# Performance work log

Hardware: AMD Instinct MI355X
Metric: run time of the kernel (lower is better)

## Reference

```python
import jax, jax.numpy as jnp
import numpy as np

B, T, S, D, V = 8, 64, 512, 512, 50000


def setup_inputs() -> dict:
    key = jax.random.key(0)
    k1, k2, k3, k4, k5 = jax.random.split(key, 5)
    x = jax.random.normal(k1, (B, T, D), dtype=jnp.float32)
    attn_dist = jax.random.normal(k2, (B, T, S), dtype=jnp.float32)
    enc_batch_extend_vocab = jax.random.randint(k3, (B, S), 0, V, dtype=jnp.int64)
    W_proj = jax.random.normal(k4, (D, V), dtype=jnp.float32) * (1.0 / np.sqrt(D))
    b_proj = jnp.zeros((V,), dtype=jnp.float32)
    W_pgen = jax.random.normal(k5, (D, 1), dtype=jnp.float32) * (1.0 / np.sqrt(D))
    b_pgen = jnp.zeros((1,), dtype=jnp.float32)
    return {"x": x, "attn_dist": attn_dist,
            "enc_batch_extend_vocab": enc_batch_extend_vocab,
            "W_proj": W_proj, "b_proj": b_proj,
            "W_pgen": W_pgen, "b_pgen": b_pgen}


def reference(x, attn_dist, enc_batch_extend_vocab, W_proj, b_proj, W_pgen, b_pgen):
    # pointer-generator head, temp=1, beam_search=False
    temp = 1.0
    # p_gen gate: [B, T, 1]
    alpha = jax.nn.sigmoid(jnp.einsum('btd,de->bte', x, W_pgen) + b_pgen)
    # vocab projection + softmax: [B, T, V]
    logit = jnp.einsum('btd,dv->btv', x, W_proj) + b_proj
    vocab_dist = jax.nn.softmax(logit / temp, axis=2)
    vocab_dist_ = alpha * vocab_dist
    # copy distribution over source positions: [B, T, S]
    attn = jax.nn.softmax(attn_dist / temp, axis=-1)
    attn_ = (1.0 - alpha) * attn
    # scatter_add copy probs into vocab dim (index broadcast over T)
    b_idx = jnp.arange(B)[:, None, None]        # [B,1,1]
    t_idx = jnp.arange(T)[None, :, None]        # [1,T,1]
    v_idx = enc_batch_extend_vocab[:, None, :]  # [B,1,S]
    merged = vocab_dist_.at[b_idx, t_idx, v_idx].add(attn_)
    return jnp.log(merged)
```

## Files before the change

kernel.cpp:

```cpp
#include <hip/hip_runtime.h>
#include <math.h>
#include <stdint.h>

#define B_ 8
#define T_ 64
#define S_ 512
#define D_ 512
#define V_ 50000
#define VP_ 50176
#define M_ (B_*T_)
#define ROWB_ ((size_t)V_ * 4)

typedef __bf16 bf16_t;
typedef bf16_t bf16x8 __attribute__((ext_vector_type(8)));
typedef float  f32x4  __attribute__((ext_vector_type(4)));

__device__ inline float blk_sum(float v, float* sm) {
    #pragma unroll
    for (int o = 32; o > 0; o >>= 1) v += __shfl_down(v, o);
    int lane = threadIdx.x & 63, wid = threadIdx.x >> 6;
    __syncthreads();
    if (lane == 0) sm[wid] = v;
    __syncthreads();
    return sm[0] + sm[1] + sm[2] + sm[3];
}

__device__ inline float blk_max(float v, float* sm) {
    #pragma unroll
    for (int o = 32; o > 0; o >>= 1) v = fmaxf(v, __shfl_down(v, o));
    int lane = threadIdx.x & 63, wid = threadIdx.x >> 6;
    __syncthreads();
    if (lane == 0) sm[wid] = v;
    __syncthreads();
    return fmaxf(fmaxf(sm[0], sm[1]), fmaxf(sm[2], sm[3]));
}

__device__ inline void unpack8(uint4 u, float f[8]) {
    uint32_t w0 = u.x, w1 = u.y, w2 = u.z, w3 = u.w;
    f[0] = __uint_as_float(w0 << 16); f[1] = __uint_as_float(w0 & 0xffff0000u);
    f[2] = __uint_as_float(w1 << 16); f[3] = __uint_as_float(w1 & 0xffff0000u);
    f[4] = __uint_as_float(w2 << 16); f[5] = __uint_as_float(w2 & 0xffff0000u);
    f[6] = __uint_as_float(w3 << 16); f[7] = __uint_as_float(w3 & 0xffff0000u);
}

__global__ __launch_bounds__(256) void kprep(
    const float* __restrict__ x, const float* __restrict__ attn_dist,
    const float* __restrict__ W_pgen, const float* __restrict__ b_pgen,
    float* __restrict__ logalpha_out, float* __restrict__ attn_out, bf16_t* __restrict__ xb,
    const int* __restrict__ idx, int* __restrict__ owner_g)
{
    __shared__ int shb[S_];
    int bid = blockIdx.x;
    int tid = threadIdx.x;

    if (bid < M_) {
        float* sm = reinterpret_cast<float*>(shb);
        int row = bid;

        float2 xv = reinterpret_cast<const float2*>(x + (size_t)row * D_)[tid];
        float2 wv = reinterpret_cast<const float2*>(W_pgen)[tid];
        union { bf16_t h[2]; uint32_t u; } pk;
        pk.h[0] = (bf16_t)xv.x; pk.h[1] = (bf16_t)xv.y;
        reinterpret_cast<uint32_t*>(xb + (size_t)row * D_)[tid] = pk.u;

        float dot = blk_sum(xv.x * wv.x + xv.y * wv.y, sm);
        float alpha = 1.f / (1.f + expf(-(dot + b_pgen[0])));
        if (tid == 0) logalpha_out[row] = logf(alpha);

        float a0 = attn_dist[(size_t)row * S_ + tid];
        float a1 = attn_dist[(size_t)row * S_ + tid + 256];
        float mx = blk_max(fmaxf(a0, a1), sm);
        float e0 = expf(a0 - mx), e1 = expf(a1 - mx);
        float s = blk_sum(e0 + e1, sm);
        float scale = (1.f - alpha) / s;
        attn_out[(size_t)row * S_ + tid]       = e0 * scale;
        attn_out[(size_t)row * S_ + tid + 256] = e1 * scale;
    } else {
        int b = bid - M_;
        for (int s = tid; s < S_; s += 256) shb[s] = idx[b * S_ + s];
        __syncthreads();
        for (int s = tid; s < S_; s += 256) {
            int v = shb[s], o = s;
            for (int s2 = 0; s2 < s; s2++) if (shb[s2] == v) { o = s2; break; }
            owner_g[b * S_ + s] = o;
        }
    }
}

#define GBM 128
#define GBN 128
#define GBK 32
#define NTK_ 16
#define BP_ 132

__global__ __launch_bounds__(256) void k2_mfma(
    const bf16_t* __restrict__ A, const float* __restrict__ W,
    const float* __restrict__ bias, char* __restrict__ outB)
{
    __shared__ bf16_t As[2][GBM][GBK];
    __shared__ __attribute__((aligned(16))) float Bf[2][GBK * BP_];
    int tid  = threadIdx.x;
    int lane = tid & 63;
    int w    = tid >> 6;
    int wm   = w >> 1, wn = w & 1;

    int bid = blockIdx.x;
    int q = bid >> 5, r = bid & 31;
    int bn = (q * 8 + (r & 7)) * GBN;
    int bm = (r >> 3) * GBM;

    f32x4 acc[4][4] = {};
    float4 wreg[4];

#define STAGE_A(BUF, K0)                                                               \
    {                                                                                  \
        _Pragma("unroll")                                                              \
        for (int i = 0; i < 2; i++) {                                                  \
            int e = (w * 2 + i) * 512 + lane * 8;                                      \
            int rr_ = e >> 5, c = e & 31;                                              \
            __builtin_amdgcn_global_load_lds(                                          \
                (const __attribute__((address_space(1))) void*)                        \
                    &A[(size_t)(bm + rr_) * D_ + (K0) + c],                            \
                (__attribute__((address_space(3))) void*)&As[BUF][(w * 2 + i) * 16][0],\
                16, 0, 0);                                                             \
        }                                                                              \
    }

#define LOAD_B(K0)                                                                     \
    {                                                                                  \
        _Pragma("unroll")                                                              \
        for (int p = 0; p < 4; p++) {                                                  \
            int i = p * 256 + tid;                                        \
            int rr_ = i >> 5;                                         \
            int c4 = i & 31;                                           \
            int gv = bn + c4 * 4;                                                      \
            wreg[p] = (gv < V_) ? *reinterpret_cast<const float4*>(                    \
                                      &W[(size_t)((K0) + rr_) * V_ + gv])              \
                                : make_float4(0.f, 0.f, 0.f, 0.f);                     \
        }                                                                              \
    }

#define WRITE_B(BUF)                                                                   \
    {                                                                                  \
        _Pragma("unroll")                                                              \
        for (int p = 0; p < 4; p++) {                                                  \
            int i = p * 256 + tid;                                                     \
            int rr_ = i >> 5;                                                          \
            int c4 = i & 31;                                                           \
            int sl = c4 ^ ((rr_ >> 3) << 2);                                           \
            *reinterpret_cast<float4*>(&Bf[BUF][rr_ * BP_ + sl * 4]) = wreg[p];        \
        }                                                                              \
    }

#define COMPUTE(BUF)                                                                   \
    {                                                                                  \
        bf16x8 af[4], bfr[4];                                                          \
        int kb = (lane >> 4) * 8;                                                      \
        int key = ((kb >> 3) << 2);              \
        _Pragma("unroll")                                                              \
        for (int mi = 0; mi < 4; mi++)                                                 \
            af[mi] = *reinterpret_cast<const bf16x8*>(                                 \
                &As[BUF][wm * 64 + mi * 16 + (lane & 15)][kb]);                        \
        _Pragma("unroll")                                                              \
        for (int ni = 0; ni < 4; ni++) {                                               \
            int n = wn * 64 + ni * 16 + (lane & 15);                                   \
            int sladdr = ((n >> 2) ^ key) * 4 + (n & 3);                               \
            bf16x8 bb;                                                                 \
            _Pragma("unroll")                                                          \
            for (int j = 0; j < 8; j++)                                                \
                bb[j] = (bf16_t)Bf[BUF][(kb + j) * BP_ + sladdr];                      \
            bfr[ni] = bb;                                                              \
        }                                                                              \
        _Pragma("unroll")                                                              \
        for (int mi = 0; mi < 4; mi++)                                                 \
            _Pragma("unroll")                                                          \
            for (int ni = 0; ni < 4; ni++)                                             \
                acc[mi][ni] = __builtin_amdgcn_mfma_f32_16x16x32_bf16(af[mi], bfr[ni], acc[mi][ni], 0, 0, 0); \
    }

    LOAD_B(0);
    STAGE_A(0, 0);
    asm volatile("s_waitcnt vmcnt(0)" ::: "memory");
    WRITE_B(0);
    __syncthreads();

    #pragma unroll
    for (int tt = 0; tt < NTK_; tt++) {
        int cur = tt & 1, nxt = cur ^ 1;
        if (tt + 1 < NTK_) {
            LOAD_B((tt + 1) * GBK);
            STAGE_A(nxt, (tt + 1) * GBK);
        }
        COMPUTE(cur);
        if (tt + 1 < NTK_) {
            asm volatile("s_waitcnt vmcnt(0)" ::: "memory");
            WRITE_B(nxt);
        }
        __syncthreads();
    }
#undef STAGE_A
#undef LOAD_B
#undef WRITE_B
#undef COMPUTE

    int cm = bm + wm * 64, cn = bn + wn * 64;
    #pragma unroll
    for (int ni = 0; ni < 4; ni++) {
        int n = cn + ni * 16 + (lane & 15);
        float bv = (n < V_) ? bias[n] : 0.f;
        #pragma unroll
        for (int mi = 0; mi < 4; mi++) {
            int rbase = cm + mi * 16 + (lane >> 4) * 4;
            #pragma unroll
            for (int rr = 0; rr < 4; rr++) {
                bf16_t val = (bf16_t)(acc[mi][ni][rr] + bv);
                *reinterpret_cast<bf16_t*>(outB + (size_t)(rbase + rr) * ROWB_ + 2 * (size_t)n) = val;
            }
        }
    }
}

#define CHUNK_ 2048
#define NCH_ ((V_ + CHUNK_ - 1) / CHUNK_)

__global__ __launch_bounds__(256) void k345_final(
    char* __restrict__ outB, const float* __restrict__ attn_, const int* __restrict__ idx,
    const int* __restrict__ owner_g, const float* __restrict__ logalpha)
{
    __shared__ float att[S_];
    __shared__ int own[S_], ids[S_];
    __shared__ float smm[4], sms[4];
    int row = blockIdx.x;
    int b = row >> 6;
    int tid = threadIdx.x;
    int lane = tid & 63, wid = tid >> 6;

    for (int s = tid; s < S_; s += 256) {
        att[s] = attn_[(size_t)row * S_ + s];
        own[s] = owner_g[b * S_ + s];
        ids[s] = idx[b * S_ + s];
    }

    const uint4* L4 = reinterpret_cast<const uint4*>(outB + (size_t)row * ROWB_);
    float m = -INFINITY, se = 0.f;
    for (int i = tid; i < V_ / 8; i += 256) {
        uint4 u = L4[i];
        float f[8]; unpack8(u, f);
        float m8 = fmaxf(fmaxf(fmaxf(f[0], f[1]), fmaxf(f[2], f[3])),
                         fmaxf(fmaxf(f[4], f[5]), fmaxf(f[6], f[7])));
        float mn = fmaxf(m, m8);
        se = se * __expf(m - mn)
           + __expf(f[0] - mn) + __expf(f[1] - mn) + __expf(f[2] - mn) + __expf(f[3] - mn)
           + __expf(f[4] - mn) + __expf(f[5] - mn) + __expf(f[6] - mn) + __expf(f[7] - mn);
        m = mn;
    }
    #pragma unroll
    for (int o = 32; o > 0; o >>= 1) {
        float m2 = __shfl_down(m, o);
        float s2 = __shfl_down(se, o);
        float mn = fmaxf(m, m2);
        if (mn == -INFINITY) { se = 0.f; }
        else se = se * __expf(m - mn) + s2 * __expf(m2 - mn);
        m = mn;
    }
    __syncthreads();
    if (lane == 0) { smm[wid] = m; sms[wid] = se; }
    __syncthreads();
    float M = smm[0], Ssum = sms[0];
    #pragma unroll
    for (int wv = 1; wv < 4; wv++) {
        float m2 = smm[wv], s2 = sms[wv];
        float mn = fmaxf(M, m2);
        if (mn != -INFINITY) Ssum = Ssum * __expf(M - mn) + s2 * __expf(m2 - mn);
        M = mn;
    }
    float logden = M + logf(Ssum);
    float c_ = logalpha[row] - logden;

    for (int s = tid; s < S_; s += 256)
        if (own[s] != s) atomicAdd(&att[own[s]], att[s]);
    __syncthreads();

    const ushort* Lrow = reinterpret_cast<const ushort*>(outB + (size_t)row * ROWB_);
    float* frow = reinterpret_cast<float*>(outB + (size_t)row * ROWB_);
    for (int c = NCH_ - 1; c >= 0; c--) {
        int i0 = c * CHUNK_ + tid * 8;
        uint4 u = make_uint4(0, 0, 0, 0);
        bool act = (i0 + 8 <= V_);
        if (act) u = *reinterpret_cast<const uint4*>(Lrow + i0);
        __syncthreads();
        if (act) {
            float f[8]; unpack8(u, f);
            float4 lo = make_float4(f[0] + c_, f[1] + c_, f[2] + c_, f[3] + c_);
            float4 hi = make_float4(f[4] + c_, f[5] + c_, f[6] + c_, f[7] + c_);
            *reinterpret_cast<float4*>(frow + i0)     = lo;
            *reinterpret_cast<float4*>(frow + i0 + 4) = hi;
        }
        __syncthreads();
    }

    for (int s = tid; s < S_; s += 256) {
        if (own[s] == s) {
            int v = ids[s];
            frow[v] = logf(expf(frow[v]) + att[s]);
        }
    }
}

__global__ __launch_bounds__(256) void k1_alpha_attn(
    const float* __restrict__ x, const float* __restrict__ attn_dist,
    const float* __restrict__ W_pgen, const float* __restrict__ b_pgen,
    float* __restrict__ logalpha_out, float* __restrict__ attn_out)
{
    __shared__ float sm[4];
    int row = blockIdx.x;
    int tid = threadIdx.x;
    float2 xv = reinterpret_cast<const float2*>(x + (size_t)row * D_)[tid];
    float2 wv = reinterpret_cast<const float2*>(W_pgen)[tid];
    float dot = blk_sum(xv.x * wv.x + xv.y * wv.y, sm);
    float alpha = 1.f / (1.f + expf(-(dot + b_pgen[0])));
    if (tid == 0) logalpha_out[row] = logf(alpha);
    float a0 = attn_dist[(size_t)row * S_ + tid];
    float a1 = attn_dist[(size_t)row * S_ + tid + 256];
    float mx = blk_max(fmaxf(a0, a1), sm);
    float e0 = expf(a0 - mx), e1 = expf(a1 - mx);
    float s = blk_sum(e0 + e1, sm);
    float scale = (1.f - alpha) / s;
    attn_out[(size_t)row * S_ + tid]       = e0 * scale;
    attn_out[(size_t)row * S_ + tid + 256] = e1 * scale;
}

__global__ __launch_bounds__(512) void k5a_owner(const int* __restrict__ idx, int* __restrict__ owner_g)
{
    __shared__ int ids[S_];
    int b = blockIdx.x;
    int s = threadIdx.x;
    ids[s] = idx[b * S_ + s];
    __syncthreads();
    int v = ids[s], o = s;
    for (int s2 = 0; s2 < s; s2++) if (ids[s2] == v) { o = s2; break; }
    owner_g[b * S_ + s] = o;
}

#define BM 64
#define BN 64
#define BK 16
__global__ __launch_bounds__(256) void k2_gemm(
    const float* __restrict__ A, const float* __restrict__ W,
    const float* __restrict__ bias, float* __restrict__ C)
{
    __shared__ float As2[BK][BM + 1];
    __shared__ float Bs2[BK][BN + 1];
    int bn = blockIdx.x * BN;
    int bm = blockIdx.y * BM;
    int tid = threadIdx.x;
    int tx = tid & 15;
    int ty = tid >> 4;
    bool full_n = (bn + BN <= V_);
    float acc[4][4] = {};
    for (int k0 = 0; k0 < D_; k0 += BK) {
        {
            int i = tid * 4;
            int row = i >> 4, col = i & 15;
            const float4 av = *reinterpret_cast<const float4*>(&A[(size_t)(bm + row) * D_ + k0 + col]);
            As2[col + 0][row] = av.x; As2[col + 1][row] = av.y;
            As2[col + 2][row] = av.z; As2[col + 3][row] = av.w;
        }
        {
            int i = tid * 4;
            int row = i >> 6, col = i & 63;
            int gn = bn + col;
            if (full_n) {
                const float4 bv = *reinterpret_cast<const float4*>(&W[(size_t)(k0 + row) * V_ + gn]);
                Bs2[row][col + 0] = bv.x; Bs2[row][col + 1] = bv.y;
                Bs2[row][col + 2] = bv.z; Bs2[row][col + 3] = bv.w;
            } else {
                #pragma unroll
                for (int j = 0; j < 4; j++)
                    Bs2[row][col + j] = (gn + j < V_) ? W[(size_t)(k0 + row) * V_ + gn + j] : 0.f;
            }
        }
        __syncthreads();
        #pragma unroll
        for (int kk = 0; kk < BK; kk++) {
            float a[4], b[4];
            #pragma unroll
            for (int i = 0; i < 4; i++) a[i] = As2[kk][ty * 4 + i];
            #pragma unroll
            for (int j = 0; j < 4; j++) b[j] = Bs2[kk][tx + j * 16];
            #pragma unroll
            for (int i = 0; i < 4; i++)
                #pragma unroll
                for (int j = 0; j < 4; j++)
                    acc[i][j] += a[i] * b[j];
        }
        __syncthreads();
    }
    #pragma unroll
    for (int i = 0; i < 4; i++) {
        int m = bm + ty * 4 + i;
        #pragma unroll
        for (int j = 0; j < 4; j++) {
            int n = bn + tx + j * 16;
            if (n < V_) C[(size_t)m * V_ + n] = acc[i][j] + bias[n];
        }
    }
}

__global__ __launch_bounds__(256) void k3_stats(const float* __restrict__ C, float* __restrict__ logden)
{
    __shared__ float smm[4], sms[4];
    int row = blockIdx.x;
    const float4* p = reinterpret_cast<const float4*>(C + (size_t)row * V_);
    float m = -INFINITY, s = 0.f;
    for (int i = threadIdx.x; i < V_ / 4; i += 256) {
        float4 v = p[i];
        float m4 = fmaxf(fmaxf(v.x, v.y), fmaxf(v.z, v.w));
        if (m4 > m) { s *= expf(m - m4); m = m4; }
        s += expf(v.x - m) + expf(v.y - m) + expf(v.z - m) + expf(v.w - m);
    }
    #pragma unroll
    for (int o = 32; o > 0; o >>= 1) {
        float m2 = __shfl_down(m, o);
        float s2 = __shfl_down(s, o);
        float mn = fmaxf(m, m2);
        s = s * expf(m - mn) + s2 * expf(m2 - mn);
        m = mn;
    }
    int lane = threadIdx.x & 63, wid = threadIdx.x >> 6;
    if (lane == 0) { smm[wid] = m; sms[wid] = s; }
    __syncthreads();
    if (threadIdx.x == 0) {
        float M = smm[0], S = sms[0];
        #pragma unroll
        for (int wv = 1; wv < 4; wv++) {
            float m2 = smm[wv], s2 = sms[wv];
            float mn = fmaxf(M, m2);
            S = S * expf(M - mn) + s2 * expf(m2 - mn);
            M = mn;
        }
        logden[row] = M + logf(S);
    }
}

__global__ __launch_bounds__(256) void k4_scale(
    float* __restrict__ C, const float* __restrict__ logalpha, const float* __restrict__ logden)
{
    int row = blockIdx.y;
    int i = blockIdx.x * 256 + threadIdx.x;
    if (i >= V_ / 4) return;
    float c_ = logalpha[row] - logden[row];
    float4* p = reinterpret_cast<float4*>(C + (size_t)row * V_) + i;
    float4 v = *p;
    v.x += c_; v.y += c_; v.z += c_; v.w += c_;
    *p = v;
}

__global__ __launch_bounds__(256) void k5_scatter_log(
    float* __restrict__ C, const float* __restrict__ attn_, const int* __restrict__ idx,
    const int* __restrict__ owner_g)
{
    __shared__ float att[S_];
    __shared__ int own[S_], ids[S_];
    int row = blockIdx.x;
    int b = row >> 6;
    int tid = threadIdx.x;
    for (int s = tid; s < S_; s += 256) {
        att[s] = attn_[(size_t)row * S_ + s];
        own[s] = owner_g[b * S_ + s];
        ids[s] = idx[b * S_ + s];
    }
    __syncthreads();
    for (int s = tid; s < S_; s += 256)
        if (own[s] != s) atomicAdd(&att[own[s]], att[s]);
    __syncthreads();
    for (int s = tid; s < S_; s += 256) {
        if (own[s] == s) {
            int v = ids[s];
            float* p = &C[(size_t)row * V_ + v];
            *p = logf(expf(*p) + att[s]);
        }
    }
}

extern "C" void kernel_launch(void* const* d_in, const int* in_sizes, int n_in,
                              void* d_out, int out_size, void* d_ws, size_t ws_size,
                              hipStream_t stream) {
    const float* x         = (const float*)d_in[0];
    const float* attn_dist = (const float*)d_in[1];
    const int*   ebev      = (const int*)  d_in[2];
    const float* W_proj    = (const float*)d_in[3];
    const float* b_proj    = (const float*)d_in[4];
    const float* W_pgen    = (const float*)d_in[5];
    const float* b_pgen    = (const float*)d_in[6];
    float* out = (float*)d_out;
    char*  outB = (char*)d_out;

    float*  logalpha = (float*)d_ws;
    float*  logden   = logalpha + M_;
    float*  attn_    = logden + M_;
    int*    owner    = (int*)(attn_ + (size_t)B_ * T_ * S_);
    bf16_t* xb       = (bf16_t*)(owner + (size_t)B_ * S_);
    size_t need = (size_t)(2 * M_ + B_ * T_ * S_ + B_ * S_) * 4
                + (size_t)M_ * D_ * 2;

    if (ws_size >= need) {
        kprep<<<M_ + B_, 256, 0, stream>>>(
            x, attn_dist, W_pgen, b_pgen, logalpha, attn_, xb, ebev, owner);

        k2_mfma<<<(VP_ / GBN) * (M_ / GBM), 256, 0, stream>>>(xb, W_proj, b_proj, outB);

        k345_final<<<M_, 256, 0, stream>>>(outB, attn_, ebev, owner, logalpha);
    } else {
        k1_alpha_attn<<<M_, 256, 0, stream>>>(x, attn_dist, W_pgen, b_pgen, logalpha, attn_);
        k5a_owner<<<B_, 512, 0, stream>>>(ebev, owner);
        dim3 g2((V_ + BN - 1) / BN, M_ / BM);
        k2_gemm<<<g2, 256, 0, stream>>>(x, W_proj, b_proj, out);
        k3_stats<<<M_, 256, 0, stream>>>(out, logden);
        dim3 g4((V_ / 4 + 255) / 256, M_);
        k4_scale<<<g4, 256, 0, stream>>>(out, logalpha, logden);
        k5_scatter_log<<<M_, 256, 0, stream>>>(out, attn_, ebev, owner);
    }
}
```

Before: 186.2 us.

## Store B tile as transposed bf16 in LDS with XOR swizzle

The W tile is now converted to bf16 once when written to shared memory and stored n-major (transposed) with an XOR swizzle, instead of being kept as fp32 k-major and converted element by element in the inner compute loop. Each thread loads four consecutive k rows for the same columns so it can pack four bf16 values per 8-byte store. The compute loop reads B fragments with two 8-byte LDS loads rather than eight scalar fp32 loads plus conversions. This halves B-tile LDS footprint and cuts LDS read instructions, at the cost of narrower global load coalescing pattern and more pack work in the write stage.

```diff
diff --git a/kernel.cpp b/kernel.cpp
--- a/kernel.cpp
+++ b/kernel.cpp
@@ -91,14 +91,13 @@
 #define GBN 128
 #define GBK 32
 #define NTK_ 16
-#define BP_ 132
 
 __global__ __launch_bounds__(256) void k2_mfma(
     const bf16_t* __restrict__ A, const float* __restrict__ W,
     const float* __restrict__ bias, char* __restrict__ outB)
 {
     __shared__ bf16_t As[2][GBM][GBK];
-    __shared__ __attribute__((aligned(16))) float Bf[2][GBK * BP_];
+    __shared__ bf16_t Bs[2][GBN * GBK];
     int tid  = threadIdx.x;
     int lane = tid & 63;
     int w    = tid >> 6;
@@ -108,6 +107,11 @@
     int q = bid >> 5, r = bid & 31;
     int bn = (q * 8 + (r & 7)) * GBN;
     int bm = (r >> 3) * GBM;
+
+    int kq  = tid >> 5;
+    int c4w = tid & 31;
+    int gv  = bn + c4w * 4;
+    bool vok = (gv < V_);
 
     f32x4 acc[4][4] = {};
     float4 wreg[4];
@@ -129,26 +133,24 @@
 #define LOAD_B(K0)                                                                     \
     {                                                                                  \
         _Pragma("unroll")                                                              \
-        for (int p = 0; p < 4; p++) {                                                  \
-            int i = p * 256 + tid;                                        \
-            int rr_ = i >> 5;                                         \
-            int c4 = i & 31;                                           \
-            int gv = bn + c4 * 4;                                                      \
-            wreg[p] = (gv < V_) ? *reinterpret_cast<const float4*>(                    \
-                                      &W[(size_t)((K0) + rr_) * V_ + gv])              \
-                                : make_float4(0.f, 0.f, 0.f, 0.f);                     \
-        }                                                                              \
+        for (int p = 0; p < 4; p++)                                                    \
+            wreg[p] = vok ? *reinterpret_cast<const float4*>(                          \
+                                &W[(size_t)((K0) + kq * 4 + p) * V_ + gv])             \
+                          : make_float4(0.f, 0.f, 0.f, 0.f);                           \
     }
 
 #define WRITE_B(BUF)                                                                   \
     {                                                                                  \
+        int sl = (kq ^ (c4w & 7)) * 4;                                                 \
         _Pragma("unroll")                                                              \
-        for (int p = 0; p < 4; p++) {                                                  \
-            int i = p * 256 + tid;                                                     \
-            int rr_ = i >> 5;                                                          \
-            int c4 = i & 31;                                                           \
-            int sl = c4 ^ ((rr_ >> 3) << 2);                                           \
-            *reinterpret_cast<float4*>(&Bf[BUF][rr_ * BP_ + sl * 4]) = wreg[p];        \
+        for (int j = 0; j < 4; j++) {                                                  \
+            int n = c4w * 4 + j;                                                       \
+            union { bf16_t h[4]; uint2 u; } pk;                                        \
+            pk.h[0] = (bf16_t)(reinterpret_cast<const float*>(&wreg[0])[j]);           \
+            pk.h[1] = (bf16_t)(reinterpret_cast<const float*>(&wreg[1])[j]);           \
+            pk.h[2] = (bf16_t)(reinterpret_cast<const float*>(&wreg[2])[j]);           \
+            pk.h[3] = (bf16_t)(reinterpret_cast<const float*>(&wreg[3])[j]);           \
+            *reinterpret_cast<uint2*>(&Bs[BUF][n * GBK + sl]) = pk.u;                  \
         }                                                                              \
     }
 
@@ -156,7 +158,7 @@
     {                                                                                  \
         bf16x8 af[4], bfr[4];                                                          \
         int kb = (lane >> 4) * 8;                                                      \
-        int key = ((kb >> 3) << 2);              \
+        int s0 = (lane >> 4) * 2;                                                      \
         _Pragma("unroll")                                                              \
         for (int mi = 0; mi < 4; mi++)                                                 \
             af[mi] = *reinterpret_cast<const bf16x8*>(                                 \
@@ -164,12 +166,12 @@
         _Pragma("unroll")                                                              \
         for (int ni = 0; ni < 4; ni++) {                                               \
             int n = wn * 64 + ni * 16 + (lane & 15);                                   \
-            int sladdr = ((n >> 2) ^ key) * 4 + (n & 3);                               \
-            bf16x8 bb;                                                                 \
-            _Pragma("unroll")                                                          \
-            for (int j = 0; j < 8; j++)                                                \
-                bb[j] = (bf16_t)Bf[BUF][(kb + j) * BP_ + sladdr];                      \
-            bfr[ni] = bb;                                                              \
+            int key = (n >> 2) & 7;                                                    \
+            uint2 lo = *reinterpret_cast<const uint2*>(&Bs[BUF][n * GBK + ((s0) ^ key) * 4]);     \
+            uint2 hi = *reinterpret_cast<const uint2*>(&Bs[BUF][n * GBK + ((s0 + 1) ^ key) * 4]); \
+            union { uint32_t u[4]; bf16x8 v; } uu;                                     \
+            uu.u[0] = lo.x; uu.u[1] = lo.y; uu.u[2] = hi.x; uu.u[3] = hi.y;            \
+            bfr[ni] = uu.v;                                                            \
         }                                                                              \
         _Pragma("unroll")                                                              \
         for (int mi = 0; mi < 4; mi++)                                                 \
```

New measurement: 240.6 us. 1.29x slower.
